# Kernel optimization log

Hardware: AMD Instinct MI355X
Metric: run time of the kernel (lower is better)

Reference implementation:

```python
import jax, jax.numpy as jnp
import numpy as np

EPS = 1.1920929e-07  # torch.finfo(float32).eps (nn.RMSNorm default eps=None)
ROPE_BASE = 10000.0


def _rmsnorm(x, g):
    # x: (..., d). torch nn.RMSNorm: x * rsqrt(mean(x^2) + eps) * g
    var = jnp.mean(jnp.square(x), axis=-1, keepdims=True)
    return x * jax.lax.rsqrt(var + EPS) * g


def _rope(x):
    # x: (b, h, s, d). Matches RotaryPositionEmbedding: half-split concat layout.
    s, d = x.shape[2], x.shape[3]
    pos = jnp.arange(s, dtype=x.dtype)[:, None]                      # (s,1)
    freqs = ROPE_BASE ** (-jnp.arange(0, d, 2, dtype=x.dtype) / d)   # (d/2,)
    ang = pos * freqs                                                # (s, d/2)
    c, sn = jnp.cos(ang), jnp.sin(ang)
    xe, xo = x[..., ::2], x[..., 1::2]
    return jnp.concatenate([xe * c - xo * sn, xe * sn + xo * c], axis=-1)


def setup_inputs() -> dict:
    key = jax.random.key(0)
    ks = jax.random.split(key, 9)
    B, S, D, F = 1, 2048, 4096, 11008
    W = 0.02  # weight scale to keep activations sane
    return {
        "x": jax.random.normal(ks[0], (B, S, D), jnp.float32),
        "wq": jax.random.normal(ks[1], (D, D), jnp.float32) * W,
        "wk": jax.random.normal(ks[2], (D, D), jnp.float32) * W,
        "wv": jax.random.normal(ks[3], (D, D), jnp.float32) * W,
        "wo": jax.random.normal(ks[4], (D, D), jnp.float32) * W,
        "w1": jax.random.normal(ks[5], (D, F), jnp.float32) * W,
        "w2": jax.random.normal(ks[6], (F, D), jnp.float32) * W,
        "w3": jax.random.normal(ks[7], (D, F), jnp.float32) * W,
        "g_attn": jnp.ones((D,), jnp.float32),
        "g_ffn": jnp.ones((D,), jnp.float32),
    }


def reference(x, wq, wk, wv, wo, w1, w2, w3, g_attn, g_ffn):
    n_heads = 32
    bsz, seqlen, dim = x.shape
    head_dim = dim // n_heads

    h = _rmsnorm(x, g_attn)
    # (b,s,d) @ (d,d) -> (b,s,h,hd) -> (b,h,s,hd)
    xq = (h @ wq).reshape(bsz, seqlen, n_heads, head_dim).transpose(0, 2, 1, 3)
    xk = (h @ wk).reshape(bsz, seqlen, n_heads, head_dim).transpose(0, 2, 1, 3)
    xv = (h @ wv).reshape(bsz, seqlen, n_heads, head_dim).transpose(0, 2, 1, 3)

    xq = _rope(xq)
    xk = _rope(xk)

    # NOTE: faithful to source: NO 1/sqrt(head_dim) scaling, NO causal mask.
    scores = jnp.einsum("bhqd,bhkd->bhqk", xq, xk)
    scores = jax.nn.softmax(scores, axis=-1)
    out = jnp.einsum("bhqk,bhkd->bhqd", scores, xv)        # (b,h,s,hd)
    out = out.transpose(0, 2, 1, 3).reshape(bsz, seqlen, dim)
    xo = out @ wo

    # NOTE: faithful to source: no residual connections; silu on w3 branch.
    h2 = _rmsnorm(xo, g_ffn)
    x1 = h2 @ w1
    x3 = jax.nn.silu(h2 @ w3)
    return (x1 * x3) @ w2
```

## Files before the change

kernel.cpp:

```cpp
#include <hip/hip_runtime.h>
#include <math.h>

typedef unsigned short u16;
typedef short short8 __attribute__((ext_vector_type(8)));
typedef float f32x4 __attribute__((ext_vector_type(4)));

#define DEV static __device__ __forceinline__

DEV float bf2f(u16 h) { union { unsigned int u; float f; } v; v.u = ((unsigned int)h) << 16; return v.f; }
DEV u16 f2bf(float f) {
  union { float f; unsigned int u; } v; v.f = f;
  unsigned int r = v.u + 0x7FFFu + ((v.u >> 16) & 1u);
  return (u16)(r >> 16);
}

DEV void gl_lds16(const void* g, void* l) {
  __builtin_amdgcn_global_load_lds(
      (const __attribute__((address_space(1))) unsigned int*)g,
      (__attribute__((address_space(3))) unsigned int*)l, 16, 0, 0);
}

template <int N> DEV void vm_wait() {
  if constexpr (N == 0) asm volatile("s_waitcnt vmcnt(0)" ::: "memory");
  else if constexpr (N == 6) asm volatile("s_waitcnt vmcnt(6)" ::: "memory");
  else if constexpr (N == 8) asm volatile("s_waitcnt vmcnt(8)" ::: "memory");
  else static_assert(N == 0 || N == 6 || N == 8, "add literal");
}

DEV void lgkm0_pin() {
  asm volatile("s_waitcnt lgkmcnt(0)" ::: "memory");
  __builtin_amdgcn_sched_barrier(0);
}

DEV void xcd_swizzle(int& bx, int& by) {
  int gx = gridDim.x, gy = gridDim.y;
  int lin = by * gx + bx;
  int xcd = lin & 7, i = lin >> 3;
  if ((gx & 7) == 0) {
    int cx = gx >> 3;
    bx = xcd * cx + i % cx;
    by = i / cx;
  } else {
    int cpx = (gx * gy) >> 3;
    int swz = xcd * cpx + i;
    bx = swz % gx;
    by = swz / gx;
  }
}

template <bool SPLIT>
__global__ __launch_bounds__(256) void rmsnorm_kernel(
    const float* __restrict__ x, const float* __restrict__ g,
    u16* __restrict__ oh, u16* __restrict__ ol) {
  int row = blockIdx.x, t = threadIdx.x;
  const float* xr = x + (size_t)row * 4096;
  float4 vals[4];
  float s = 0.f;
#pragma unroll
  for (int i = 0; i < 4; i++) {
    vals[i] = ((const float4*)xr)[t + i * 256];
    s += vals[i].x * vals[i].x + vals[i].y * vals[i].y + vals[i].z * vals[i].z + vals[i].w * vals[i].w;
  }
#pragma unroll
  for (int m = 1; m < 64; m <<= 1) s += __shfl_xor(s, m);
  __shared__ float red[4];
  if ((t & 63) == 0) red[t >> 6] = s;
  __syncthreads();
  s = red[0] + red[1] + red[2] + red[3];
  float rinv = rsqrtf(s * (1.f / 4096.f) + 1.1920929e-07f);
#pragma unroll
  for (int i = 0; i < 4; i++) {
    float4 gv = ((const float4*)g)[t + i * 256];
    float4 v = vals[i];
    float f[4] = {v.x * rinv * gv.x, v.y * rinv * gv.y, v.z * rinv * gv.z, v.w * rinv * gv.w};
    ushort4 rh, rl;
    u16* hp = (u16*)&rh; u16* lp = (u16*)&rl;
#pragma unroll
    for (int j = 0; j < 4; j++) {
      u16 hi = f2bf(f[j]);
      hp[j] = hi;
      if (SPLIT) lp[j] = f2bf(f[j] - bf2f(hi));
    }
    ((ushort4*)(oh + (size_t)row * 4096))[t + i * 256] = rh;
    if (SPLIT) ((ushort4*)(ol + (size_t)row * 4096))[t + i * 256] = rl;
  }
}

__global__ void tconv_kernel(const float* __restrict__ in, u16* __restrict__ out, int K, int N) {
  __shared__ float tile[32][33];
  int k0 = blockIdx.y * 32, n0 = blockIdx.x * 32;
  int tx = threadIdx.x, ty = threadIdx.y;
#pragma unroll
  for (int i = 0; i < 4; i++)
    tile[ty + 8 * i][tx] = in[(size_t)(k0 + ty + 8 * i) * N + n0 + tx];
  __syncthreads();
#pragma unroll
  for (int i = 0; i < 4; i++) {
    int n = ty + 8 * i;
    out[(size_t)(n0 + n) * K + k0 + tx] = f2bf(tile[tx][n]);
  }
}

__global__ void tconv_ilv_kernel(const float* __restrict__ in, u16* __restrict__ out,
                                 int K, int N, int off) {
  __shared__ float tile[32][33];
  int k0 = blockIdx.y * 32, n0 = blockIdx.x * 32;
  int tx = threadIdx.x, ty = threadIdx.y;
#pragma unroll
  for (int i = 0; i < 4; i++)
    tile[ty + 8 * i][tx] = in[(size_t)(k0 + ty + 8 * i) * N + n0 + tx];
  __syncthreads();
#pragma unroll
  for (int i = 0; i < 4; i++) {
    int n = n0 + ty + 8 * i;
    int orow = ((n >> 7) << 8) + (n & 127) + off;
    out[(size_t)orow * K + k0 + tx] = f2bf(tile[tx][ty + 8 * i]);
  }
}

__global__ void tconv_split_kernel(const float* __restrict__ in, u16* __restrict__ oh,
                                   u16* __restrict__ ol, int K, int N) {
  __shared__ float tile[32][33];
  int k0 = blockIdx.y * 32, n0 = blockIdx.x * 32;
  int tx = threadIdx.x, ty = threadIdx.y;
#pragma unroll
  for (int i = 0; i < 4; i++)
    tile[ty + 8 * i][tx] = in[(size_t)(k0 + ty + 8 * i) * N + n0 + tx];
  __syncthreads();
#pragma unroll
  for (int i = 0; i < 4; i++) {
    int n = ty + 8 * i;
    float f = tile[tx][n];
    u16 hi = f2bf(f);
    size_t idx = (size_t)(n0 + n) * K + k0 + tx;
    oh[idx] = hi;
    ol[idx] = f2bf(f - bf2f(hi));
  }
}

__global__ __launch_bounds__(256) void rope_table_kernel(float* __restrict__ tab) {
  int i = blockIdx.x * 256 + threadIdx.x;
  int j = i & 63, s = i >> 6;
  double freq = pow(10000.0, -(double)j / 64.0);
  double ang = (double)s * freq;
  tab[i * 2] = (float)cos(ang);
  tab[i * 2 + 1] = (float)sin(ang);
}

__global__ __launch_bounds__(256) void rope_inplace_kernel(
    u16* hi, u16* lo, const float* __restrict__ tab) {
  int idx = blockIdx.x * 256 + threadIdx.x;
  int j = idx & 63, hd = (idx >> 6) & 63, s = idx >> 12;
  size_t base = (size_t)s * 8192 + hd * 128;
  float xe = bf2f(hi[base + 2 * j]) + bf2f(lo[base + 2 * j]);
  float xo = bf2f(hi[base + 2 * j + 1]) + bf2f(lo[base + 2 * j + 1]);
  float cs = tab[(s * 64 + j) * 2], sn = tab[(s * 64 + j) * 2 + 1];
  float r0 = xe * cs - xo * sn;
  float r1 = xe * sn + xo * cs;
  u16 h0 = f2bf(r0), h1 = f2bf(r1);
  hi[base + j] = h0;      lo[base + j] = f2bf(r0 - bf2f(h0));
  hi[base + 64 + j] = h1; lo[base + 64 + j] = f2bf(r1 - bf2f(h1));
}

template <int OUT, bool TRIK>
__global__ __launch_bounds__(512, 2) void gemm8_kernel(
    const u16* __restrict__ A, const u16* __restrict__ A2,
    const u16* __restrict__ B, const u16* __restrict__ B2,
    void* __restrict__ C, u16* __restrict__ C2,
    int M, int N, int K, int lda, int ldb) {
  __shared__ __attribute__((aligned(16))) u16 SMEM[65536];
  int t = threadIdx.x, l = t & 63, w = t >> 6;
  int bx = blockIdx.x, by = blockIdx.y;
  xcd_swizzle(bx, by);
  int m0 = by * 256, n0 = bx * 256;
  int wm = w >> 2, wn = w & 3, bh = wn >> 1;
  f32x4 acc[8][4] = {};
  int nk = K >> 6;

  auto AsP = [&](int d, int h) -> u16* { return SMEM + (d * 2 + h) * 8192; };
  auto BsP = [&](int d, int h) -> u16* { return SMEM + 32768 + (d * 2 + h) * 8192; };

  auto stageA = [&](int kt, int dd) {
    const u16* Ab = A; int kc = kt << 6;
    if (TRIK) { int seg = kt >> 6; Ab = (seg == 1) ? A2 : A; kc = (kt & 63) << 6; }
#pragma unroll
    for (int i = 0; i < 4; i++) {
      int id = i * 512 + t;
      int hh = id >> 10, idc = id & 1023;
      int r = idc >> 3, cb = idc & 7;
      int csw = ((cb * 16) ^ ((r & 7) << 4)) >> 1;
      gl_lds16(&Ab[(size_t)(m0 + hh * 128 + r) * lda + kc + csw], AsP(dd, hh) + idc * 8);
    }
  };
  auto stageB = [&](int kt, int dd) {
    const u16* Bb = B; int kc = kt << 6;
    if (TRIK) { int seg = kt >> 6; Bb = (seg == 2) ? B2 : B; kc = (kt & 63) << 6; }
#pragma unroll
    for (int i = 0; i < 4; i++) {
      int id = i * 512 + t;
      int hh = id >> 10, idc = id & 1023;
      int r = idc >> 3, cb = idc & 7;
      int csw = ((cb * 16) ^ ((r & 7) << 4)) >> 1;
      gl_lds16(&Bb[(size_t)(n0 + hh * 128 + r) * ldb + kc + csw], BsP(dd, hh) + idc * 8);
    }
  };

  int lq = l >> 4, lr = l & 15;
  short8 af[4][2], bf[4][2];
  auto rdA = [&](int d, int mh) {
    const char* Ax = (const char*)AsP(d, wm);
#pragma unroll
    for (int m = 0; m < 4; m++) {
      int r = mh * 64 + m * 16 + lr;
      int rb = r * 128, rx = (r & 7) << 4;
#pragma unroll
      for (int kh = 0; kh < 2; kh++)
        af[m][kh] = *(const short8*)(Ax + rb + ((kh * 64 + lq * 16) ^ rx));
    }
  };
  auto rdB2 = [&](int d, int nlo, int nhi) {
    const char* Bx = (const char*)BsP(d, bh);
#pragma unroll
    for (int n = 0; n < 4; n++) {
      if (n < nlo || n >= nhi) continue;
      int r = (wn & 1) * 64 + n * 16 + lr;
      int rb = r * 128, rx = (r & 7) << 4;
#pragma unroll
      for (int kh = 0; kh < 2; kh++)
        bf[n][kh] = *(const short8*)(Bx + rb + ((kh * 64 + lq * 16) ^ rx));
    }
  };
  auto mm8 = [&](int mo, int no) {
    __builtin_amdgcn_s_setprio(1);
#pragma unroll
    for (int m = 0; m < 4; m++)
#pragma unroll
      for (int n = 0; n < 2; n++)
#pragma unroll
        for (int kh = 0; kh < 2; kh++)
          acc[mo + m][no + n] =
              __builtin_amdgcn_mfma_f32_16x16x32_bf16(af[m][kh], bf[no + n][kh], acc[mo + m][no + n], 0, 0, 0);
    __builtin_amdgcn_s_setprio(0);
  };

  stageB(0, 0); stageA(0, 0);
  stageB(1, 1); stageA(1, 1);
  vm_wait<8>();
  __builtin_amdgcn_s_barrier();

  for (int kt = 0; kt < nk; ++kt) {
    int d = kt & 1;
    rdA(d, 0);
    rdB2(d, 0, 2);
    __builtin_amdgcn_s_barrier();
    lgkm0_pin();
    mm8(0, 0);
    __builtin_amdgcn_s_barrier();
    rdB2(d, 2, 4);
    __builtin_amdgcn_s_barrier();
    lgkm0_pin();
    mm8(0, 2);
    __builtin_amdgcn_s_barrier();
    rdA(d, 1);
    if (kt + 2 < nk) stageB(kt + 2, d);
    __builtin_amdgcn_s_barrier();
    lgkm0_pin();
    mm8(4, 2);
    __builtin_amdgcn_s_barrier();
    if (kt + 2 < nk) stageA(kt + 2, d);
    __builtin_amdgcn_s_barrier();
    mm8(4, 0);
    if (kt + 2 < nk) vm_wait<8>();
    else vm_wait<0>();
    __builtin_amdgcn_s_barrier();
  }

  if (OUT == 3) {
    __syncthreads();
    float* EPI = (float*)SMEM;
    if (wn >= 2) {
#pragma unroll
      for (int m = 0; m < 8; m++)
#pragma unroll
        for (int i = 0; i < 4; i++) {
          int rl = wm * 128 + m * 16 + lq * 4 + i;
#pragma unroll
          for (int n = 0; n < 4; n++)
            EPI[rl * 128 + (wn - 2) * 64 + n * 16 + lr] = acc[m][n][i];
        }
    }
    __syncthreads();
    if (wn < 2) {
      u16* Ob = (u16*)C;
      int cb = n0 >> 1;
#pragma unroll
      for (int m = 0; m < 8; m++)
#pragma unroll
        for (int i = 0; i < 4; i++) {
          int rl = wm * 128 + m * 16 + lq * 4 + i;
          int row = m0 + rl;
#pragma unroll
          for (int n = 0; n < 4; n++) {
            float a = acc[m][n][i];
            float b = EPI[rl * 128 + wn * 64 + n * 16 + lr];
            float r = a * (b / (1.f + expf(-b)));
            Ob[(size_t)row * N + cb + wn * 64 + n * 16 + lr] = f2bf(r);
          }
        }
    }
    return;
  }

#pragma unroll
  for (int m = 0; m < 8; m++) {
#pragma unroll
    for (int i = 0; i < 4; i++) {
      int row = m0 + wm * 128 + m * 16 + lq * 4 + i;
      size_t rb = (size_t)row * N + n0 + wn * 64 + lr;
#pragma unroll
      for (int n = 0; n < 4; n++) {
        float f = acc[m][n][i];
        if (OUT == 0) ((float*)C)[rb + n * 16] = f;
        else if (OUT == 1) ((u16*)C)[rb + n * 16] = f2bf(f);
        else {
          u16 hi = f2bf(f);
          ((u16*)C)[rb + n * 16] = hi;
          C2[rb + n * 16] = f2bf(f - bf2f(hi));
        }
      }
    }
  }
}

template <int OUT>
__global__ __launch_bounds__(512, 2) void gemm8n_kernel(
    const u16* __restrict__ A, const u16* __restrict__ B, void* __restrict__ C,
    int M, int N, int K, int lda, int ldb) {
  __shared__ __attribute__((aligned(16))) u16 As[2][128 * 64];
  __shared__ __attribute__((aligned(16))) u16 Bs3[3][256 * 64];
  int t = threadIdx.x, l = t & 63, w = t >> 6;
  int bx = blockIdx.x, by = blockIdx.y;
  xcd_swizzle(bx, by);
  int m0 = by * 128, n0 = bx * 256;
  int wm = w >> 2, wn = w & 3;
  f32x4 acc[4][4] = {};
  int nk = K >> 6;

  auto stageA = [&](int kt, int dd) {
    int kc = kt << 6;
#pragma unroll
    for (int i = 0; i < 2; i++) {
      int id = i * 512 + t;
      int r = id >> 3, cb = id & 7;
      int csw = ((cb * 16) ^ ((r & 7) << 4)) >> 1;
      gl_lds16(&A[(size_t)(m0 + r) * lda + kc + csw], &As[dd][id * 8]);
    }
  };
  auto stageB = [&](int kt, int bb) {
    int kc = kt << 6;
#pragma unroll
    for (int i = 0; i < 4; i++) {
      int id = i * 512 + t;
      int r = id >> 3, cb = id & 7;
      int csw = ((cb * 16) ^ ((r & 7) << 4)) >> 1;
      gl_lds16(&B[(size_t)(n0 + r) * ldb + kc + csw], &Bs3[bb][id * 8]);
    }
  };

  int lq = l >> 4, lr = l & 15;
  short8 af0[4], af1[4], bf0[4], bf1[4];
  auto rdA4 = [&](short8 (&dst)[4], int d, int kh) {
    const char* Ax = (const char*)As[d];
#pragma unroll
    for (int m = 0; m < 4; m++) {
      int r = wm * 64 + m * 16 + lr;
      dst[m] = *(const short8*)(Ax + r * 128 + ((kh * 64 + lq * 16) ^ ((r & 7) << 4)));
    }
  };
  auto rdB4 = [&](short8 (&dst)[4], int bb, int kh) {
    const char* Bx = (const char*)Bs3[bb];
#pragma unroll
    for (int n = 0; n < 4; n++) {
      int r = wn * 64 + n * 16 + lr;
      dst[n] = *(const short8*)(Bx + r * 128 + ((kh * 64 + lq * 16) ^ ((r & 7) << 4)));
    }
  };
  auto mm16 = [&](short8 (&a)[4], short8 (&b)[4]) {
    __builtin_amdgcn_s_setprio(1);
#pragma unroll
    for (int m = 0; m < 4; m++)
#pragma unroll
      for (int n = 0; n < 4; n++)
        acc[m][n] = __builtin_amdgcn_mfma_f32_16x16x32_bf16(a[m], b[n], acc[m][n], 0, 0, 0);
    __builtin_amdgcn_s_setprio(0);
  };

  stageB(0, 0); stageA(0, 0);
  stageB(1, 1); stageA(1, 1);
  vm_wait<6>();
  __builtin_amdgcn_s_barrier();

  for (int kt = 0; kt < nk; ++kt) {
    int d = kt & 1;
    int bb = kt % 3, bb2 = (kt + 2) % 3;
    if (kt + 2 < nk) stageB(kt + 2, bb2);
    rdA4(af0, d, 0); rdB4(bf0, bb, 0);
    __builtin_amdgcn_s_barrier();
    lgkm0_pin();
    mm16(af0, bf0);
    __builtin_amdgcn_s_barrier();
    rdA4(af1, d, 1); rdB4(bf1, bb, 1);
    lgkm0_pin();
    __builtin_amdgcn_s_barrier();
    if (kt + 2 < nk) { stageA(kt + 2, d); vm_wait<6>(); }
    else vm_wait<0>();
    mm16(af1, bf1);
    __builtin_amdgcn_s_barrier();
  }
  if (OUT == 2) {
    u16* Cb = (u16*)C;
#pragma unroll
    for (int m = 0; m < 4; m++) {
      int sbase = m0 + wm * 64 + m * 16 + lq * 4;
#pragma unroll
      for (int n = 0; n < 4; n++) {
        int dg = n0 + wn * 64 + n * 16 + lr;
        ushort4 pk;
        pk.x = f2bf(acc[m][n][0]); pk.y = f2bf(acc[m][n][1]);
        pk.z = f2bf(acc[m][n][2]); pk.w = f2bf(acc[m][n][3]);
        *(ushort4*)&Cb[(size_t)dg * M + sbase] = pk;
      }
    }
    return;
  }
#pragma unroll
  for (int m = 0; m < 4; m++) {
#pragma unroll
    for (int i = 0; i < 4; i++) {
      int row = m0 + wm * 64 + m * 16 + lq * 4 + i;
      size_t rb = (size_t)row * N + n0 + wn * 64 + lr;
#pragma unroll
      for (int n = 0; n < 4; n++) {
        float f = acc[m][n][i];
        if (OUT == 0) ((float*)C)[rb + n * 16] = f;
        else ((u16*)C)[rb + n * 16] = f2bf(f);
      }
    }
  }
}

__global__ __launch_bounds__(256) void attn_kernel(
    const u16* __restrict__ qh, const u16* __restrict__ ql,
    const u16* __restrict__ kh, const u16* __restrict__ kl,
    const u16* __restrict__ vt, u16* __restrict__ out) {
  const int QS = 8192;
  __shared__ __attribute__((aligned(16))) u16 KH[64 * 128];
  __shared__ __attribute__((aligned(16))) u16 KL[64 * 128];
  __shared__ __attribute__((aligned(16))) u16 Vl[128 * 64];
  __shared__ __attribute__((aligned(16))) u16 Pl[4][16 * 72];
  int t = threadIdx.x, l = t & 63, w = t >> 6;
  int hd = blockIdx.y, q0 = blockIdx.x * 64;
  int qrow = q0 + w * 16 + (l & 15);
  size_t qoff = (size_t)qrow * QS + hd * 128 + (l >> 4) * 8;
  short8 qfh[4], qfl[4];
#pragma unroll
  for (int kc = 0; kc < 4; kc++) {
    qfh[kc] = *(const short8*)&qh[qoff + kc * 32];
    qfl[kc] = *(const short8*)&ql[qoff + kc * 32];
  }
  f32x4 accO[8] = {};
  float mrun = -__builtin_inff(), lrun = 0.f;
  for (int kv0 = 0; kv0 < 2048; kv0 += 64) {
#pragma unroll
    for (int i = 0; i < 4; i++) {
      int ci = i * 256 + t;
      int row = ci >> 4;
      int cb = (ci & 15) ^ (row & 7);
      size_t src = (size_t)(kv0 + row) * QS + hd * 128 + cb * 8;
      gl_lds16(&kh[src], &KH[ci * 8]);
      gl_lds16(&kl[src], &KL[ci * 8]);
    }
#pragma unroll
    for (int i = 0; i < 4; i++) {
      int ci = i * 256 + t;
      int row = ci >> 3;
      int cb = (ci & 7) ^ (row & 7);
      gl_lds16(&vt[((size_t)hd * 128 + row) * 2048 + kv0 + cb * 8], &Vl[ci * 8]);
    }
    __syncthreads();
    f32x4 accS[4];
#pragma unroll
    for (int mm = 0; mm < 4; mm++) {
      accS[mm] = (f32x4){0.f, 0.f, 0.f, 0.f};
#pragma unroll
      for (int kc = 0; kc < 4; kc++) {
        int rowk = mm * 16 + (l & 15);
        int logb = rowk * 256 + kc * 64 + (l >> 4) * 16;
        int phys = logb ^ ((rowk & 7) << 4);
        short8 a_h = *(const short8*)((const char*)KH + phys);
        short8 a_l = *(const short8*)((const char*)KL + phys);
        accS[mm] = __builtin_amdgcn_mfma_f32_16x16x32_bf16(a_h, qfh[kc], accS[mm], 0, 0, 0);
        accS[mm] = __builtin_amdgcn_mfma_f32_16x16x32_bf16(a_h, qfl[kc], accS[mm], 0, 0, 0);
        accS[mm] = __builtin_amdgcn_mfma_f32_16x16x32_bf16(a_l, qfh[kc], accS[mm], 0, 0, 0);
      }
    }
    float tmax = -__builtin_inff();
#pragma unroll
    for (int mm = 0; mm < 4; mm++)
      tmax = fmaxf(tmax, fmaxf(fmaxf(accS[mm][0], accS[mm][1]), fmaxf(accS[mm][2], accS[mm][3])));
    tmax = fmaxf(tmax, __shfl_xor(tmax, 16));
    tmax = fmaxf(tmax, __shfl_xor(tmax, 32));
    float mnew = fmaxf(mrun, tmax);
    float scale = expf(mrun - mnew);
    float psum = 0.f;
#pragma unroll
    for (int mm = 0; mm < 4; mm++) {
      float p0 = expf(accS[mm][0] - mnew), p1 = expf(accS[mm][1] - mnew);
      float p2 = expf(accS[mm][2] - mnew), p3 = expf(accS[mm][3] - mnew);
      psum += (p0 + p1) + (p2 + p3);
      ushort4 pk;
      pk.x = f2bf(p0); pk.y = f2bf(p1); pk.z = f2bf(p2); pk.w = f2bf(p3);
      *(ushort4*)&Pl[w][(l & 15) * 72 + mm * 16 + (l >> 4) * 4] = pk;
    }
    psum += __shfl_xor(psum, 16);
    psum += __shfl_xor(psum, 32);
    lrun = lrun * scale + psum;
    mrun = mnew;
#pragma unroll
    for (int mm = 0; mm < 8; mm++) accO[mm] = accO[mm] * scale;
#pragma unroll
    for (int kc2 = 0; kc2 < 2; kc2++) {
      short8 bp = *(const short8*)((const char*)&Pl[w][0] + (l & 15) * 144 + kc2 * 64 + (l >> 4) * 16);
#pragma unroll
      for (int mm = 0; mm < 8; mm++) {
        int rowd = mm * 16 + (l & 15);
        int logb = rowd * 128 + kc2 * 64 + (l >> 4) * 16;
        int phys = logb ^ ((rowd & 7) << 4);
        short8 av = *(const short8*)((const char*)Vl + phys);
        accO[mm] = __builtin_amdgcn_mfma_f32_16x16x32_bf16(av, bp, accO[mm], 0, 0, 0);
      }
    }
    __syncthreads();
  }
  float rinv = 1.f / lrun;
#pragma unroll
  for (int mm = 0; mm < 8; mm++) {
    ushort4 pk;
    pk.x = f2bf(accO[mm][0] * rinv); pk.y = f2bf(accO[mm][1] * rinv);
    pk.z = f2bf(accO[mm][2] * rinv); pk.w = f2bf(accO[mm][3] * rinv);
    *(ushort4*)&out[(size_t)qrow * 4096 + hd * 128 + mm * 16 + (l >> 4) * 4] = pk;
  }
}

extern "C" void kernel_launch(void* const* d_in, const int* in_sizes, int n_in,
                              void* d_out, int out_size, void* d_ws, size_t ws_size,
                              hipStream_t stream) {
  const float* x      = (const float*)d_in[0];
  const float* wq     = (const float*)d_in[1];
  const float* wk     = (const float*)d_in[2];
  const float* wv     = (const float*)d_in[3];
  const float* wo     = (const float*)d_in[4];
  const float* w1     = (const float*)d_in[5];
  const float* w2     = (const float*)d_in[6];
  const float* w3     = (const float*)d_in[7];
  const float* g_attn = (const float*)d_in[8];
  const float* g_ffn  = (const float*)d_in[9];

  char* ws = (char*)d_ws;
  char* R0 = ws;
  char* R1 = R0 + (size_t)22016 * 4096 * 2;
  char* R2 = R1 + (size_t)8192 * 4096 * 2;
  char* R3 = R2 + (size_t)2 * 2048 * 4096 * 2;
  char* R4 = R3 + (size_t)2 * 2048 * 8192 * 2;
  char* RT = R4 + (size_t)2 * 2048 * 4096 * 2;
  (void)ws_size; (void)in_sizes; (void)n_in; (void)out_size;

  u16* wA     = (u16*)R0;
  u16* wB     = (u16*)R1;
  u16* h_hi   = (u16*)R2;
  u16* h_lo   = (u16*)(R2 + (size_t)2048 * 4096 * 2);
  u16* qk_hi  = (u16*)R3;
  u16* qk_lo  = (u16*)(R3 + (size_t)2048 * 8192 * 2);
  u16* ao     = (u16*)R4;
  u16* vT     = (u16*)(R4 + (size_t)2048 * 4096 * 2);
  float* xo   = (float*)R1;
  u16* h2     = (u16*)(R1 + (size_t)2048 * 4096 * 4);
  u16* x1silu = (u16*)R3;
  float* tab  = (float*)RT;

  dim3 tb(32, 8);
  dim3 g44(4096 / 32, 4096 / 32);

  rope_table_kernel<<<512, 256, 0, stream>>>(tab);
  rmsnorm_kernel<true><<<2048, 256, 0, stream>>>(x, g_attn, h_hi, h_lo);
  tconv_split_kernel<<<g44, tb, 0, stream>>>(wq, wA, wB, 4096, 4096);
  tconv_split_kernel<<<g44, tb, 0, stream>>>(wk, wA + (size_t)4096 * 4096, wB + (size_t)4096 * 4096, 4096, 4096);
  gemm8_kernel<2, true><<<dim3(32, 8), 512, 0, stream>>>(
      h_hi, h_lo, wA, wB, qk_hi, qk_lo, 2048, 8192, 12288, 4096, 4096);
  rope_inplace_kernel<<<32768, 256, 0, stream>>>(qk_hi, qk_lo, tab);
  tconv_kernel<<<g44, tb, 0, stream>>>(wv, wA, 4096, 4096);
  gemm8n_kernel<2><<<dim3(16, 16), 512, 0, stream>>>(h_hi, wA, vT, 2048, 4096, 4096, 4096, 4096);
  attn_kernel<<<dim3(32, 32), 256, 0, stream>>>(qk_hi, qk_lo, qk_hi + 4096, qk_lo + 4096, vT, ao);
  tconv_kernel<<<g44, tb, 0, stream>>>(wo, wA, 4096, 4096);
  gemm8n_kernel<0><<<dim3(16, 16), 512, 0, stream>>>(ao, wA, xo, 2048, 4096, 4096, 4096, 4096);
  rmsnorm_kernel<false><<<2048, 256, 0, stream>>>(xo, g_ffn, h2, nullptr);
  tconv_ilv_kernel<<<dim3(344, 128), tb, 0, stream>>>(w1, wA, 4096, 11008, 0);
  tconv_ilv_kernel<<<dim3(344, 128), tb, 0, stream>>>(w3, wA, 4096, 11008, 128);
  gemm8_kernel<3, false><<<dim3(86, 8), 512, 0, stream>>>(
      h2, nullptr, wA, nullptr, x1silu, nullptr, 2048, 11008, 4096, 4096, 4096);
  tconv_kernel<<<dim3(128, 344), tb, 0, stream>>>(w2, wA, 11008, 4096);
  gemm8n_kernel<0><<<dim3(16, 16), 512, 0, stream>>>(x1silu, wA, (float*)d_out, 2048, 4096, 11008, 11008, 11008);
}
```

Baseline: 1.696 ms.

## Widen transpose-convert tiles and route split-precision QK GEMM through gemm8n kernel

The weight transpose/convert kernels now process 64x64 tiles with float2 loads and ushort2 stores instead of 32x32 scalar accesses, to cut launch count and improve memory access width. The gemm8n kernel gains a TRIK mode that walks three K segments (hi*hi, lo*hi, hi*lo) over split operands and a hi/lo split output. The QK projection moves onto this kernel with a 128x256 tile and 512 blocks, replacing the earlier gemm8 kernel. An unused SiLU-gated epilogue (OUT==4) is also added, along with a single flat LDS buffer.

```diff
diff --git a/kernel.cpp b/kernel.cpp
--- a/kernel.cpp
+++ b/kernel.cpp
@@ -87,54 +87,76 @@
 }
 
 __global__ void tconv_kernel(const float* __restrict__ in, u16* __restrict__ out, int K, int N) {
-  __shared__ float tile[32][33];
-  int k0 = blockIdx.y * 32, n0 = blockIdx.x * 32;
+  __shared__ float tile[64][65];
+  int k0 = blockIdx.y * 64, n0 = blockIdx.x * 64;
   int tx = threadIdx.x, ty = threadIdx.y;
 #pragma unroll
-  for (int i = 0; i < 4; i++)
-    tile[ty + 8 * i][tx] = in[(size_t)(k0 + ty + 8 * i) * N + n0 + tx];
+  for (int i = 0; i < 8; i++) {
+    int r = ty + 8 * i;
+    float2 v = *(const float2*)&in[(size_t)(k0 + r) * N + n0 + tx * 2];
+    tile[r][tx * 2] = v.x;
+    tile[r][tx * 2 + 1] = v.y;
+  }
   __syncthreads();
 #pragma unroll
-  for (int i = 0; i < 4; i++) {
-    int n = ty + 8 * i;
-    out[(size_t)(n0 + n) * K + k0 + tx] = f2bf(tile[tx][n]);
+  for (int i = 0; i < 8; i++) {
+    int c = ty + 8 * i;
+    ushort2 o;
+    o.x = f2bf(tile[tx * 2][c]);
+    o.y = f2bf(tile[tx * 2 + 1][c]);
+    *(ushort2*)&out[(size_t)(n0 + c) * K + k0 + tx * 2] = o;
   }
 }
 
 __global__ void tconv_ilv_kernel(const float* __restrict__ in, u16* __restrict__ out,
                                  int K, int N, int off) {
-  __shared__ float tile[32][33];
-  int k0 = blockIdx.y * 32, n0 = blockIdx.x * 32;
+  __shared__ float tile[64][65];
+  int k0 = blockIdx.y * 64, n0 = blockIdx.x * 64;
   int tx = threadIdx.x, ty = threadIdx.y;
 #pragma unroll
-  for (int i = 0; i < 4; i++)
-    tile[ty + 8 * i][tx] = in[(size_t)(k0 + ty + 8 * i) * N + n0 + tx];
+  for (int i = 0; i < 8; i++) {
+    int r = ty + 8 * i;
+    float2 v = *(const float2*)&in[(size_t)(k0 + r) * N + n0 + tx * 2];
+    tile[r][tx * 2] = v.x;
+    tile[r][tx * 2 + 1] = v.y;
+  }
   __syncthreads();
 #pragma unroll
-  for (int i = 0; i < 4; i++) {
-    int n = n0 + ty + 8 * i;
+  for (int i = 0; i < 8; i++) {
+    int c = ty + 8 * i;
+    int n = n0 + c;
     int orow = ((n >> 7) << 8) + (n & 127) + off;
-    out[(size_t)orow * K + k0 + tx] = f2bf(tile[tx][ty + 8 * i]);
+    ushort2 o;
+    o.x = f2bf(tile[tx * 2][c]);
+    o.y = f2bf(tile[tx * 2 + 1][c]);
+    *(ushort2*)&out[(size_t)orow * K + k0 + tx * 2] = o;
   }
 }
 
 __global__ void tconv_split_kernel(const float* __restrict__ in, u16* __restrict__ oh,
                                    u16* __restrict__ ol, int K, int N) {
-  __shared__ float tile[32][33];
-  int k0 = blockIdx.y * 32, n0 = blockIdx.x * 32;
+  __shared__ float tile[64][65];
+  int k0 = blockIdx.y * 64, n0 = blockIdx.x * 64;
   int tx = threadIdx.x, ty = threadIdx.y;
 #pragma unroll
-  for (int i = 0; i < 4; i++)
-    tile[ty + 8 * i][tx] = in[(size_t)(k0 + ty + 8 * i) * N + n0 + tx];
+  for (int i = 0; i < 8; i++) {
+    int r = ty + 8 * i;
+    float2 v = *(const float2*)&in[(size_t)(k0 + r) * N + n0 + tx * 2];
+    tile[r][tx * 2] = v.x;
+    tile[r][tx * 2 + 1] = v.y;
+  }
   __syncthreads();
 #pragma unroll
-  for (int i = 0; i < 4; i++) {
-    int n = ty + 8 * i;
-    float f = tile[tx][n];
-    u16 hi = f2bf(f);
-    size_t idx = (size_t)(n0 + n) * K + k0 + tx;
-    oh[idx] = hi;
-    ol[idx] = f2bf(f - bf2f(hi));
+  for (int i = 0; i < 8; i++) {
+    int c = ty + 8 * i;
+    float f0 = tile[tx * 2][c], f1 = tile[tx * 2 + 1][c];
+    u16 h0 = f2bf(f0), h1 = f2bf(f1);
+    ushort2 vh, vl;
+    vh.x = h0; vh.y = h1;
+    vl.x = f2bf(f0 - bf2f(h0)); vl.y = f2bf(f1 - bf2f(h1));
+    size_t idx = (size_t)(n0 + c) * K + k0 + tx * 2;
+    *(ushort2*)&oh[idx] = vh;
+    *(ushort2*)&ol[idx] = vl;
   }
 }
 
@@ -332,12 +354,13 @@
   }
 }
 
-template <int OUT>
+template <int OUT, bool TRIK>
 __global__ __launch_bounds__(512, 2) void gemm8n_kernel(
-    const u16* __restrict__ A, const u16* __restrict__ B, void* __restrict__ C,
+    const u16* __restrict__ A, const u16* __restrict__ A2,
+    const u16* __restrict__ B, const u16* __restrict__ B2,
+    void* __restrict__ C, u16* __restrict__ C2,
     int M, int N, int K, int lda, int ldb) {
-  __shared__ __attribute__((aligned(16))) u16 As[2][128 * 64];
-  __shared__ __attribute__((aligned(16))) u16 Bs3[3][256 * 64];
+  __shared__ __attribute__((aligned(16))) u16 SMEM[65536];
   int t = threadIdx.x, l = t & 63, w = t >> 6;
   int bx = blockIdx.x, by = blockIdx.y;
   xcd_swizzle(bx, by);
@@ -346,31 +369,36 @@
   f32x4 acc[4][4] = {};
   int nk = K >> 6;
 
+  auto AsP = [&](int d) -> u16* { return SMEM + d * 8192; };
+  auto BsP = [&](int b) -> u16* { return SMEM + 16384 + b * 16384; };
+
   auto stageA = [&](int kt, int dd) {
-    int kc = kt << 6;
+    const u16* Ab = A; int kc = kt << 6;
+    if (TRIK) { int seg = kt >> 6; Ab = (seg == 1) ? A2 : A; kc = (kt & 63) << 6; }
 #pragma unroll
     for (int i = 0; i < 2; i++) {
       int id = i * 512 + t;
       int r = id >> 3, cb = id & 7;
       int csw = ((cb * 16) ^ ((r & 7) << 4)) >> 1;
-      gl_lds16(&A[(size_t)(m0 + r) * lda + kc + csw], &As[dd][id * 8]);
+      gl_lds16(&Ab[(size_t)(m0 + r) * lda + kc + csw], AsP(dd) + id * 8);
     }
   };
   auto stageB = [&](int kt, int bb) {
-    int kc = kt << 6;
+    const u16* Bb = B; int kc = kt << 6;
+    if (TRIK) { int seg = kt >> 6; Bb = (seg == 2) ? B2 : B; kc = (kt & 63) << 6; }
 #pragma unroll
     for (int i = 0; i < 4; i++) {
       int id = i * 512 + t;
       int r = id >> 3, cb = id & 7;
       int csw = ((cb * 16) ^ ((r & 7) << 4)) >> 1;
-      gl_lds16(&B[(size_t)(n0 + r) * ldb + kc + csw], &Bs3[bb][id * 8]);
+      gl_lds16(&Bb[(size_t)(n0 + r) * ldb + kc + csw], BsP(bb) + id * 8);
     }
   };
 
   int lq = l >> 4, lr = l & 15;
   short8 af0[4], af1[4], bf0[4], bf1[4];
   auto rdA4 = [&](short8 (&dst)[4], int d, int kh) {
-    const char* Ax = (const char*)As[d];
+    const char* Ax = (const char*)AsP(d);
 #pragma unroll
     for (int m = 0; m < 4; m++) {
       int r = wm * 64 + m * 16 + lr;
@@ -378,7 +406,7 @@
     }
   };
   auto rdB4 = [&](short8 (&dst)[4], int bb, int kh) {
-    const char* Bx = (const char*)Bs3[bb];
+    const char* Bx = (const char*)BsP(bb);
 #pragma unroll
     for (int n = 0; n < 4; n++) {
       int r = wn * 64 + n * 16 + lr;
@@ -417,6 +445,7 @@
     mm16(af1, bf1);
     __builtin_amdgcn_s_barrier();
   }
+
   if (OUT == 2) {
     u16* Cb = (u16*)C;
 #pragma unroll
@@ -433,6 +462,41 @@
     }
     return;
   }
+  if (OUT == 4) {
+    __syncthreads();
+    float* EPI = (float*)SMEM;
+    if (wn >= 2) {
+#pragma unroll
+      for (int m = 0; m < 4; m++)
+#pragma unroll
+        for (int i = 0; i < 4; i++) {
+          int rl = wm * 64 + m * 16 + lq * 4 + i;
+#pragma unroll
+          for (int n = 0; n < 4; n++)
+            EPI[rl * 128 + (wn - 2) * 64 + n * 16 + lr] = acc[m][n][i];
+        }
+    }
+    __syncthreads();
+    if (wn < 2) {
+      u16* Ob = (u16*)C;
+      int cb = n0 >> 1;
+#pragma unroll
+      for (int m = 0; m < 4; m++)
+#pragma unroll
+        for (int i = 0; i < 4; i++) {
+          int rl = wm * 64 + m * 16 + lq * 4 + i;
+          int row = m0 + rl;
+#pragma unroll
+          for (int n = 0; n < 4; n++) {
+            float a = acc[m][n][i];
+            float b = EPI[rl * 128 + wn * 64 + n * 16 + lr];
+            float r = a * (b / (1.f + expf(-b)));
+            Ob[(size_t)row * N + cb + wn * 64 + n * 16 + lr] = f2bf(r);
+          }
+        }
+    }
+    return;
+  }
 #pragma unroll
   for (int m = 0; m < 4; m++) {
 #pragma unroll
@@ -443,7 +507,12 @@
       for (int n = 0; n < 4; n++) {
         float f = acc[m][n][i];
         if (OUT == 0) ((float*)C)[rb + n * 16] = f;
-        else ((u16*)C)[rb + n * 16] = f2bf(f);
+        else if (OUT == 1) ((u16*)C)[rb + n * 16] = f2bf(f);
+        else {
+          u16 hi = f2bf(f);
+          ((u16*)C)[rb + n * 16] = hi;
+          C2[rb + n * 16] = f2bf(f - bf2f(hi));
+        }
       }
     }
   }
@@ -589,25 +658,27 @@
   float* tab  = (float*)RT;
 
   dim3 tb(32, 8);
-  dim3 g44(4096 / 32, 4096 / 32);
 
   rope_table_kernel<<<512, 256, 0, stream>>>(tab);
   rmsnorm_kernel<true><<<2048, 256, 0, stream>>>(x, g_attn, h_hi, h_lo);
-  tconv_split_kernel<<<g44, tb, 0, stream>>>(wq, wA, wB, 4096, 4096);
-  tconv_split_kernel<<<g44, tb, 0, stream>>>(wk, wA + (size_t)4096 * 4096, wB + (size_t)4096 * 4096, 4096, 4096);
-  gemm8_kernel<2, true><<<dim3(32, 8), 512, 0, stream>>>(
+  tconv_split_kernel<<<dim3(64, 64), tb, 0, stream>>>(wq, wA, wB, 4096, 4096);
+  tconv_split_kernel<<<dim3(64, 64), tb, 0, stream>>>(wk, wA + (size_t)4096 * 4096, wB + (size_t)4096 * 4096, 4096, 4096);
+  gemm8n_kernel<3, true><<<dim3(32, 16), 512, 0, stream>>>(
       h_hi, h_lo, wA, wB, qk_hi, qk_lo, 2048, 8192, 12288, 4096, 4096);
   rope_inplace_kernel<<<32768, 256, 0, stream>>>(qk_hi, qk_lo, tab);
-  tconv_kernel<<<g44, tb, 0, stream>>>(wv, wA, 4096, 4096);
-  gemm8n_kernel<2><<<dim3(16, 16), 512, 0, stream>>>(h_hi, wA, vT, 2048, 4096, 4096, 4096, 4096);
+  tconv_kernel<<<dim3(64, 64), tb, 0, stream>>>(wv, wA, 4096, 4096);
+  gemm8n_kernel<2, false><<<dim3(16, 16), 512, 0, stream>>>(
+      h_hi, nullptr, wA, nullptr, vT, nullptr, 2048, 4096, 4096, 4096, 4096);
   attn_kernel<<<dim3(32, 32), 256, 0, stream>>>(qk_hi, qk_lo, qk_hi + 4096, qk_lo + 4096, vT, ao);
-  tconv_kernel<<<g44, tb, 0, stream>>>(wo, wA, 4096, 4096);
-  gemm8n_kernel<0><<<dim3(16, 16), 512, 0, stream>>>(ao, wA, xo, 2048, 4096, 4096, 4096, 4096);
+  tconv_kernel<<<dim3(64, 64), tb, 0, stream>>>(wo, wA, 4096, 4096);
+  gemm8n_kernel<0, false><<<dim3(16, 16), 512, 0, stream>>>(
+      ao, nullptr, wA, nullptr, xo, nullptr, 2048, 4096, 4096, 4096, 4096);
   rmsnorm_kernel<false><<<2048, 256, 0, stream>>>(xo, g_ffn, h2, nullptr);
-  tconv_ilv_kernel<<<dim3(344, 128), tb, 0, stream>>>(w1, wA, 4096, 11008, 0);
-  tconv_ilv_kernel<<<dim3(344, 128), tb, 0, stream>>>(w3, wA, 4096, 11008, 128);
+  tconv_ilv_kernel<<<dim3(172, 64), tb, 0, stream>>>(w1, wA, 4096, 11008, 0);
+  tconv_ilv_kernel<<<dim3(172, 64), tb, 0, stream>>>(w3, wA, 4096, 11008, 128);
   gemm8_kernel<3, false><<<dim3(86, 8), 512, 0, stream>>>(
       h2, nullptr, wA, nullptr, x1silu, nullptr, 2048, 11008, 4096, 4096, 4096);
-  tconv_kernel<<<dim3(128, 344), tb, 0, stream>>>(w2, wA, 11008, 4096);
-  gemm8n_kernel<0><<<dim3(16, 16), 512, 0, stream>>>(x1silu, wA, (float*)d_out, 2048, 4096, 11008, 11008, 11008);
-}
+  tconv_kernel<<<dim3(64, 172), tb, 0, stream>>>(w2, wA, 11008, 4096);
+  gemm8n_kernel<0, false><<<dim3(16, 16), 512, 0, stream>>>(
+      x1silu, nullptr, wA, nullptr, (float*)d_out, nullptr, 2048, 4096, 11008, 11008, 11008);
+}
```

After: 1.648 ms. 2.8% less time.
